# Performance work log

Measured on AMD Instinct MI355X. Metric: run time of the kernel, lower is better.

The kernel has to match this reference:

```python
import jax, jax.numpy as jnp
import numpy as np

B, S, D, H = 2, 2048, 2048, 16
HD = D // H


def setup_inputs() -> dict:
    key = jax.random.key(0)
    ks = jax.random.split(key, 11)
    scale = 1.0 / np.sqrt(D)
    causal = jnp.tril(jnp.ones((S, S), dtype=bool))
    attention_mask = jnp.broadcast_to(causal, (B, H, S, S))
    return {
        "queries": jax.random.normal(ks[0], (B, S, D), dtype=jnp.float32),
        "keys": jax.random.normal(ks[1], (B, S, D), dtype=jnp.float32),
        "values": jax.random.normal(ks[2], (B, S, D), dtype=jnp.float32),
        "attention_mask": attention_mask,
        "wq": jax.random.normal(ks[3], (D, D), dtype=jnp.float32) * scale,
        "bq": jax.random.normal(ks[4], (D,), dtype=jnp.float32) * 0.01,
        "wk": jax.random.normal(ks[5], (D, D), dtype=jnp.float32) * scale,
        "bk": jax.random.normal(ks[6], (D,), dtype=jnp.float32) * 0.01,
        "wv": jax.random.normal(ks[7], (D, D), dtype=jnp.float32) * scale,
        "bv": jax.random.normal(ks[8], (D,), dtype=jnp.float32) * 0.01,
        "wo": jax.random.normal(ks[9], (D, D), dtype=jnp.float32) * scale,
        "bo": jax.random.normal(ks[10], (D,), dtype=jnp.float32) * 0.01,
    }


def _split_heads(x):
    # (B, S, D) -> (B, H, S, HD)
    b, s, _ = x.shape
    return x.reshape(b, s, H, HD).transpose(0, 2, 1, 3)


def reference(queries, keys, values, attention_mask, wq, bq, wk, bk, wv, bv, wo, bo):
    # Linear layers (torch convention: x @ W.T + b)
    q = _split_heads(queries @ wq.T + bq)   # (B, H, S, HD)
    k = _split_heads(keys @ wk.T + bk)
    v = _split_heads(values @ wv.T + bv)

    inv_sqrt_d = 1.0 / jnp.sqrt(jnp.asarray(HD, dtype=q.dtype))
    scores = jnp.einsum('bhqd,bhkd->bhqk', q, k) * inv_sqrt_d  # (B, H, S, S)
    scores = jnp.where(attention_mask, scores, jnp.asarray(-jnp.inf, dtype=scores.dtype))
    probs = jax.nn.softmax(scores, axis=-1)
    out = jnp.einsum('bhqk,bhkd->bhqd', probs, v)              # (B, H, S, HD)

    out = out.transpose(0, 2, 1, 3).reshape(queries.shape[0], queries.shape[1], D)
    return out @ wo.T + bo
```

## Files before the change

kernel.cpp:

```cpp
#include <hip/hip_runtime.h>
#include <hip/hip_bf16.h>

typedef unsigned short u16;
typedef __bf16 bf16x8 __attribute__((ext_vector_type(8)));
typedef short  short8 __attribute__((ext_vector_type(8)));
typedef float  f32x4  __attribute__((ext_vector_type(4)));
typedef float  f32x16 __attribute__((ext_vector_type(16)));
typedef u16    u16x4  __attribute__((ext_vector_type(4)));
typedef unsigned uintx2 __attribute__((ext_vector_type(2)));

#define BB 2
#define SS 2048
#define DD 2048
#define HH 16
#define HDIM 128
#define MM (BB * SS)
#define KSCALE 0.12752039505554602f

static __device__ __forceinline__ f32x4 mfma16(short8 a, short8 b, f32x4 c) {
    return __builtin_amdgcn_mfma_f32_16x16x32_bf16(
        __builtin_bit_cast(bf16x8, a), __builtin_bit_cast(bf16x8, b), c, 0, 0, 0);
}

static __device__ __forceinline__ f32x16 mfma32(short8 a, short8 b, f32x16 c) {
    return __builtin_amdgcn_mfma_f32_32x32x16_bf16(
        __builtin_bit_cast(bf16x8, a), __builtin_bit_cast(bf16x8, b), c, 0, 0, 0);
}

static __device__ __forceinline__ u16 f2bf(float f) {
    union { float f; unsigned u; } v; v.f = f;
    unsigned r = v.u + 0x7fffu + ((v.u >> 16) & 1u);
    return (u16)(r >> 16);
}

static __device__ __forceinline__ float bf2f(u16 v) {
    union { unsigned u; float f; } t; t.u = ((unsigned)v) << 16;
    return t.f;
}

static __device__ __forceinline__ unsigned cvtpk(float lo, float hi) {
    unsigned r;
    asm("v_cvt_pk_bf16_f32 %0, %1, %2" : "=v"(r) : "v"(lo), "v"(hi));
    return r;
}

static __device__ __forceinline__ void plswap(unsigned &a, unsigned &b) {
    asm("v_permlane32_swap_b32 %0, %1" : "+v"(a), "+v"(b));
}

static __device__ __forceinline__ uint4 pack8(float4 a, float4 b) {
    uint4 o;
    o.x = (unsigned)f2bf(a.x) | ((unsigned)f2bf(a.y) << 16);
    o.y = (unsigned)f2bf(a.z) | ((unsigned)f2bf(a.w) << 16);
    o.z = (unsigned)f2bf(b.x) | ((unsigned)f2bf(b.y) << 16);
    o.w = (unsigned)f2bf(b.z) | ((unsigned)f2bf(b.w) << 16);
    return o;
}

static __device__ __forceinline__ void gload_lds16(const u16* g, u16* l) {
    __builtin_amdgcn_global_load_lds(
        (const __attribute__((address_space(1))) unsigned int*)g,
        (__attribute__((address_space(3))) unsigned int*)l, 16, 0, 0);
}

__global__ __launch_bounds__(256) void conv_all(
    const float* __restrict__ q, const float* __restrict__ k, const float* __restrict__ v,
    const float* __restrict__ wq, const float* __restrict__ wk,
    const float* __restrict__ wv, const float* __restrict__ wo,
    u16* __restrict__ out)
{
    constexpr int n1 = MM * DD / 8;
    constexpr int nw = DD * DD / 8;
    constexpr int total = 3 * n1 + 4 * nw;
    const int stride = gridDim.x * blockDim.x;
    for (int i = blockIdx.x * blockDim.x + threadIdx.x; i < total; i += stride) {
        const float* s; int j = i; float sc = 1.f;
        if (j < n1)            { s = q; }
        else if (j < 2 * n1)   { s = k;  j -= n1; }
        else if (j < 3 * n1)   { s = v;  j -= 2 * n1; }
        else {
            j -= 3 * n1;
            if (j < nw)        { s = wq; sc = KSCALE; }
            else if (j < 2*nw) { s = wk; j -= nw; }
            else if (j < 3*nw) { s = wv; j -= 2 * nw; }
            else               { s = wo; j -= 3 * nw; }
        }
        const float4* sp = (const float4*)s + (size_t)j * 2;
        float4 a = sp[0], bb2 = sp[1];
        a.x *= sc; a.y *= sc; a.z *= sc; a.w *= sc;
        bb2.x *= sc; bb2.y *= sc; bb2.z *= sc; bb2.w *= sc;
        ((uint4*)out)[i] = pack8(a, bb2);
    }
}

__global__ __launch_bounds__(256, 3) void gemm_qkv(
    const u16* __restrict__ A0, const u16* __restrict__ W0,
    const float* __restrict__ bq, const float* __restrict__ bk,
    const float* __restrict__ bv, u16* __restrict__ C0)
{
    __shared__ u16 S[128 * 132];
    u16* Al = S;
    u16* Bl = S + 4096;

    const int z = blockIdx.z;
    const u16* A  = A0 + (size_t)z * MM * DD;
    const u16* Wb = W0 + (size_t)z * DD * DD;
    const float* bias = (z == 0) ? bq : (z == 1 ? bk : bv);
    const float bsc = (z == 0) ? KSCALE : 1.f;

    const int tid = threadIdx.x;
    const int lane = tid & 63;
    const int lg = lane >> 4, li = lane & 15;
    const int wid = tid >> 6;
    const int brow = blockIdx.x * 128, bcol = blockIdx.y * 128;
    const int wm = wid >> 1, wn = wid & 1;

    const int srow = tid >> 2;
    const int scol = (tid & 3) * 8;

    const f32x4 zero = {0.f, 0.f, 0.f, 0.f};
    f32x4 acc[4][4];
#pragma unroll
    for (int i = 0; i < 4; ++i)
#pragma unroll
        for (int j = 0; j < 4; ++j) acc[i][j] = zero;

    const u16* aptr = A  + (size_t)(brow + srow) * DD + scol;
    const u16* bptr = Wb + (size_t)(bcol + srow) * DD + scol;
    const size_t half = (size_t)64 * DD;

    for (int kt = 0; kt < DD; kt += 32) {
        gload_lds16(aptr + kt,        &Al[tid * 8]);
        gload_lds16(aptr + half + kt, &Al[2048 + tid * 8]);
        gload_lds16(bptr + kt,        &Bl[tid * 8]);
        gload_lds16(bptr + half + kt, &Bl[2048 + tid * 8]);
        __syncthreads();

        short8 af[4], bf[4];
#pragma unroll
        for (int mi = 0; mi < 4; ++mi)
            af[mi] = *(const short8*)(&Al[(wm * 64 + mi * 16 + li) * 32 + lg * 8]);
#pragma unroll
        for (int ni = 0; ni < 4; ++ni)
            bf[ni] = *(const short8*)(&Bl[(wn * 64 + ni * 16 + li) * 32 + lg * 8]);
#pragma unroll
        for (int mi = 0; mi < 4; ++mi)
#pragma unroll
            for (int ni = 0; ni < 4; ++ni)
                acc[mi][ni] = mfma16(af[mi], bf[ni], acc[mi][ni]);
        __syncthreads();
    }

    if (z == 2) {
        u16* Cl = S;
#pragma unroll
        for (int ni = 0; ni < 4; ++ni) {
            const int cc = wn * 64 + ni * 16 + li;
            const float bvv = bias[bcol + cc];
#pragma unroll
            for (int mi = 0; mi < 4; ++mi)
#pragma unroll
                for (int r = 0; r < 4; ++r) {
                    const int rr = wm * 64 + mi * 16 + lg * 4 + r;
                    Cl[cc * 132 + rr] = f2bf(acc[mi][ni][r] + bvv);
                }
        }
        __syncthreads();
        const int row = tid >> 1;
        const int hcol = (tid & 1) * 64;
        u16* dst = C0 + (size_t)2 * MM * DD + (size_t)(bcol + row) * MM + brow + hcol;
#pragma unroll
        for (int c = 0; c < 8; ++c)
            *(short8*)(dst + c * 8) = *(const short8*)(&Cl[row * 132 + hcol + c * 8]);
    } else {
        u16* Cp = C0 + (size_t)z * MM * DD;
#pragma unroll
        for (int ni = 0; ni < 4; ++ni) {
            const int col = bcol + wn * 64 + ni * 16 + li;
            const float bvv = bias[col] * bsc;
#pragma unroll
            for (int mi = 0; mi < 4; ++mi)
#pragma unroll
                for (int r = 0; r < 4; ++r) {
                    const int row = brow + wm * 64 + mi * 16 + lg * 4 + r;
                    Cp[(size_t)row * DD + col] = f2bf(acc[mi][ni][r] + bvv);
                }
        }
    }
}

__global__ __launch_bounds__(256) void gemm_out(
    const u16* __restrict__ A, const u16* __restrict__ Wb,
    const float* __restrict__ bias, float* __restrict__ Cp)
{
    __shared__ u16 Al[128 * 32];
    __shared__ u16 Bl[128 * 32];

    const int tid = threadIdx.x;
    const int lane = tid & 63;
    const int lg = lane >> 4, li = lane & 15;
    const int wid = tid >> 6;
    const int brow = blockIdx.x * 128, bcol = blockIdx.y * 128;
    const int wm = wid >> 1, wn = wid & 1;

    const f32x4 zero = {0.f, 0.f, 0.f, 0.f};
    f32x4 acc[4][4];
#pragma unroll
    for (int i = 0; i < 4; ++i)
#pragma unroll
        for (int j = 0; j < 4; ++j) acc[i][j] = zero;

    const int srow = tid >> 2;
    const int scol = (tid & 3) * 8;
    const u16* aptr = A  + (size_t)(brow + srow) * DD + scol;
    const u16* bptr = Wb + (size_t)(bcol + srow) * DD + scol;
    const size_t half = (size_t)64 * DD;

    for (int kt = 0; kt < DD; kt += 32) {
        gload_lds16(aptr + kt,        &Al[tid * 8]);
        gload_lds16(aptr + half + kt, &Al[2048 + tid * 8]);
        gload_lds16(bptr + kt,        &Bl[tid * 8]);
        gload_lds16(bptr + half + kt, &Bl[2048 + tid * 8]);
        __syncthreads();

        short8 af[4], bf[4];
#pragma unroll
        for (int mi = 0; mi < 4; ++mi)
            af[mi] = *(const short8*)(&Al[(wm * 64 + mi * 16 + li) * 32 + lg * 8]);
#pragma unroll
        for (int ni = 0; ni < 4; ++ni)
            bf[ni] = *(const short8*)(&Bl[(wn * 64 + ni * 16 + li) * 32 + lg * 8]);
#pragma unroll
        for (int mi = 0; mi < 4; ++mi)
#pragma unroll
            for (int ni = 0; ni < 4; ++ni)
                acc[mi][ni] = mfma16(af[mi], bf[ni], acc[mi][ni]);
        __syncthreads();
    }

#pragma unroll
    for (int ni = 0; ni < 4; ++ni) {
        const int col = bcol + wn * 64 + ni * 16 + li;
        const float bvv = bias[col];
#pragma unroll
        for (int mi = 0; mi < 4; ++mi)
#pragma unroll
            for (int r = 0; r < 4; ++r) {
                const int row = brow + wm * 64 + mi * 16 + lg * 4 + r;
                Cp[(size_t)row * DD + col] = acc[mi][ni][r] + bvv;
            }
    }
}

__global__ __launch_bounds__(256) void flash_attn(
    const u16* __restrict__ Q, const u16* __restrict__ Kp,
    const u16* __restrict__ Vt, u16* __restrict__ O,
    u16* __restrict__ PartO, float* __restrict__ PartML)
{
    __shared__ u16 lds[16384];
    u16* Kl = lds;
    u16* Vl = lds + 8192;

    const int tid = threadIdx.x;
    const int wid = tid >> 6, lane = tid & 63;
    const int l5 = lane & 31;
    const int hi = lane >> 5;

    const int lin = (int)blockIdx.x + 51 * ((int)blockIdx.y + 16 * (int)blockIdx.z);
    const int xcd = lin & 7;
    const int idx = lin >> 3;
    const int grp = xcd + 8 * (idx & 3);
    const int f   = idx >> 2;
    const int b = grp >> 4, h = grp & 15;

    int qt = 15, rem = f, C;
    for (;;) { C = (2 * qt + 7) / 6; if (rem < C) break; rem -= C; --qt; }
    const int ch = rem;
    const int T = 2 * qt + 2;
    const int j0 = ch * T / C;
    const int j1 = (ch + 1) * T / C;
    const int qbase = qt * 128 + wid * 32;
    const int qg = qbase + l5;

    const int rK0 = tid >> 4, wK0 = tid & 15;
    const int bK0 = ((wK0 * 16) ^ ((rK0 & 7) << 4)) >> 1;
    const int rV0 = tid >> 3, wV0 = tid & 7;
    const int bV0 = ((wV0 * 16) ^ ((rV0 & 7) << 4)) >> 1;
    const u16* kbase = Kp + (size_t)(b * SS + rK0) * DD + h * HDIM + bK0;
    const u16* vbase = Vt + (size_t)(h * HDIM + rV0) * MM + b * SS + bV0;

    short8 qf[8];
    {
        const u16* qp0 = Q + (size_t)(b * SS + qg) * DD + h * HDIM + hi * 8;
#pragma unroll
        for (int ks = 0; ks < 8; ++ks)
            qf[ks] = *(const short8*)(qp0 + ks * 16);
    }

    float m_r = -__builtin_inff(), l_r = 0.f;
    f32x16 accO[4];
#pragma unroll
    for (int d = 0; d < 4; ++d) accO[d] = (f32x16)(0.f);

    for (int j = j0; j < j1; ++j) {
#pragma unroll
        for (int i_ = 0; i_ < 4; ++i_) {
            gload_lds16(kbase + (size_t)(j * 64 + i_ * 16) * DD, &Kl[(i_ * 256 + tid) * 8]);
            gload_lds16(vbase + (size_t)(i_ * 32) * MM + j * 64, &Vl[(i_ * 256 + tid) * 8]);
        }
        __syncthreads();

        if (j * 64 <= qbase + 31) {
            f32x16 accS[2];
            accS[0] = (f32x16)(0.f); accS[1] = (f32x16)(0.f);
            __builtin_amdgcn_s_setprio(1);
#pragma unroll
            for (int ks = 0; ks < 8; ++ks) {
#pragma unroll
                for (int kvb = 0; kvb < 2; ++kvb) {
                    const int row = kvb * 32 + l5;
                    const int e = (ks * 16 + hi * 8) ^ ((row & 7) << 3);
                    short8 kf = *(const short8*)(&Kl[row * 128 + e]);
                    accS[kvb] = mfma32(kf, qf[ks], accS[kvb]);
                }
            }
            __builtin_amdgcn_s_setprio(0);

            const bool domask = (j * 64 + 63 > qbase);
            float rmax = -__builtin_inff();
            if (domask) {
#pragma unroll
                for (int kvb = 0; kvb < 2; ++kvb)
#pragma unroll
                    for (int r = 0; r < 16; ++r) {
                        float t = accS[kvb][r];
                        const int kv = j * 64 + kvb * 32 + (r & 3) + 8 * (r >> 2) + 4 * hi;
                        if (kv > qg) t = -__builtin_inff();
                        accS[kvb][r] = t;
                        rmax = fmaxf(rmax, t);
                    }
            } else {
#pragma unroll
                for (int kvb = 0; kvb < 2; ++kvb)
#pragma unroll
                    for (int r = 0; r < 16; ++r)
                        rmax = fmaxf(rmax, accS[kvb][r]);
            }
            rmax = fmaxf(rmax, __shfl_xor(rmax, 32, 64));

            if (!__all(rmax - m_r <= 11.5f)) {
                const float mn = fmaxf(m_r, rmax);
                const float sf = exp2f(m_r - mn);
                m_r = mn;
                l_r *= sf;
#pragma unroll
                for (int db = 0; db < 4; ++db) accO[db] = accO[db] * sf;
            }

            float ls = 0.f;
#pragma unroll
            for (int kvb = 0; kvb < 2; ++kvb)
#pragma unroll
                for (int r = 0; r < 16; ++r) {
                    const float e = exp2f(accS[kvb][r] - m_r);
                    accS[kvb][r] = e;
                    ls += e;
                }
            ls += __shfl_xor(ls, 32, 64);
            l_r += ls;

            __builtin_amdgcn_s_setprio(1);
#pragma unroll
            for (int ks = 0; ks < 4; ++ks) {
                const int kvb = ks >> 1;
                const int r0 = (ks & 1) * 8;
                unsigned x0 = cvtpk(accS[kvb][r0 + 0], accS[kvb][r0 + 1]);
                unsigned y0 = cvtpk(accS[kvb][r0 + 2], accS[kvb][r0 + 3]);
                unsigned x1 = cvtpk(accS[kvb][r0 + 4], accS[kvb][r0 + 5]);
                unsigned y1 = cvtpk(accS[kvb][r0 + 6], accS[kvb][r0 + 7]);
                plswap(x0, x1);
                plswap(y0, y1);
                union { unsigned u[4]; short8 s; } pf;
                pf.u[0] = x0; pf.u[1] = y0; pf.u[2] = x1; pf.u[3] = y1;
#pragma unroll
                for (int db = 0; db < 4; ++db) {
                    const int row = db * 32 + l5;
                    const int e = (ks * 16 + hi * 8) ^ ((row & 7) << 3);
                    short8 vf = *(const short8*)(&Vl[row * 64 + e]);
                    accO[db] = mfma32(vf, pf.s, accO[db]);
                }
            }
            __builtin_amdgcn_s_setprio(0);
        }
        __syncthreads();
    }

    if (C > 1) {
        int sbase = 0;
        for (int q2 = 3; q2 < qt; ++q2) sbase += (2 * q2 + 7) / 6;
        const int pslot = grp * 48 + sbase + ch;
        u16* po = PartO + (size_t)pslot * 16384 + (size_t)(wid * 32 + l5) * 128;
#pragma unroll
        for (int db = 0; db < 4; ++db)
#pragma unroll
            for (int g = 0; g < 4; ++g) {
                const int d0 = db * 32 + g * 8 + hi * 4;
                uintx2 pk;
                pk.x = cvtpk(accO[db][g * 4 + 0], accO[db][g * 4 + 1]);
                pk.y = cvtpk(accO[db][g * 4 + 2], accO[db][g * 4 + 3]);
                *(uintx2*)(po + d0) = pk;
            }
        if (lane < 32) {
            float* ml = PartML + (size_t)pslot * 256;
            ml[wid * 32 + l5]       = m_r;
            ml[128 + wid * 32 + l5] = l_r;
        }
    } else {
        const float linv = 1.f / l_r;
        u16* Wl = lds + wid * 4096;
#pragma unroll
        for (int db = 0; db < 4; ++db)
#pragma unroll
            for (int g = 0; g < 4; ++g) {
                const int d0 = db * 32 + g * 8 + hi * 4;
                uintx2 pk;
                pk.x = cvtpk(accO[db][g * 4 + 0] * linv, accO[db][g * 4 + 1] * linv);
                pk.y = cvtpk(accO[db][g * 4 + 2] * linv, accO[db][g * 4 + 3] * linv);
                *(uintx2*)(&Wl[l5 * 128 + (d0 ^ ((l5 & 7) << 4))]) = pk;
            }
        const int q_l = lane >> 1;
        const int d0r = (lane & 1) * 64;
        u16* op = O + (size_t)(b * SS + qt * 128 + wid * 32 + q_l) * DD + h * HDIM + d0r;
#pragma unroll
        for (int c = 0; c < 8; ++c) {
            short8 vv = *(const short8*)(&Wl[q_l * 128 + ((d0r + c * 8) ^ ((q_l & 7) << 4))]);
            *(short8*)(op + c * 8) = vv;
        }
    }
}

__global__ __launch_bounds__(256) void attn_combine(
    const u16* __restrict__ PartO, const float* __restrict__ PartML,
    u16* __restrict__ O)
{
    const int qt = 3 + (int)blockIdx.x;
    const int h = blockIdx.y, b = blockIdx.z;
    const int nch = (2 * qt + 7) / 6;
    int sbase = 0;
    for (int q2 = 3; q2 < qt; ++q2) sbase += (2 * q2 + 7) / 6;
    const int pbase = (b * HH + h) * 48 + sbase;

    const int tid = threadIdx.x;
    const int q = tid & 127;
    const int d0 = (tid >> 7) * 64;

    float mc[6], lc[6];
#pragma unroll
    for (int c = 0; c < 6; ++c) {
        if (c < nch) {
            mc[c] = PartML[(size_t)(pbase + c) * 256 + q];
            lc[c] = PartML[(size_t)(pbase + c) * 256 + 128 + q];
        } else { mc[c] = -__builtin_inff(); lc[c] = 0.f; }
    }
    float M = mc[0];
#pragma unroll
    for (int c = 1; c < 6; ++c) M = fmaxf(M, mc[c]);
    float wc[6], L = 0.f;
#pragma unroll
    for (int c = 0; c < 6; ++c) { wc[c] = exp2f(mc[c] - M); L += wc[c] * lc[c]; }
    const float Linv = 1.f / L;

    float acc[64];
#pragma unroll
    for (int i = 0; i < 64; ++i) acc[i] = 0.f;
#pragma unroll
    for (int c = 0; c < 6; ++c) {
        if (c < nch) {
            const float w = wc[c] * Linv;
            const u16* po = PartO + (size_t)(pbase + c) * 16384 + (size_t)q * 128 + d0;
#pragma unroll
            for (int i = 0; i < 64; ++i)
                acc[i] += w * bf2f(po[i]);
        }
    }

    u16* op = O + (size_t)(b * SS + qt * 128 + q) * DD + h * HDIM + d0;
#pragma unroll
    for (int j = 0; j < 8; ++j) {
        short8 vv;
#pragma unroll
        for (int e = 0; e < 8; ++e) vv[e] = (short)f2bf(acc[j * 8 + e]);
        *(short8*)(op + j * 8) = vv;
    }
}

extern "C" void kernel_launch(void* const* d_in, const int* in_sizes, int n_in,
                              void* d_out, int out_size, void* d_ws, size_t ws_size,
                              hipStream_t stream)
{
    const float* queries = (const float*)d_in[0];
    const float* keys    = (const float*)d_in[1];
    const float* values  = (const float*)d_in[2];
    const float* wq = (const float*)d_in[4];
    const float* bq = (const float*)d_in[5];
    const float* wk = (const float*)d_in[6];
    const float* bk = (const float*)d_in[7];
    const float* wv = (const float*)d_in[8];
    const float* bv = (const float*)d_in[9];
    const float* wo = (const float*)d_in[10];
    const float* bo = (const float*)d_in[11];

    const int NMD = MM * DD;
    const int NWW = DD * DD;

    u16* qb  = (u16*)d_ws;
    u16* wqb = qb  + (size_t)3 * NMD;
    u16* wob = wqb + (size_t)3 * NWW;
    u16* qw  = wob + (size_t)NWW;
    u16* aw  = qw  + (size_t)3 * NMD;
    u16*   partO  = qb;
    float* partML = (float*)wqb;
    (void)in_sizes; (void)n_in; (void)out_size; (void)ws_size;

    dim3 blk(256);
    dim3 gridC(2048);
    dim3 gridQKV(MM / 128, DD / 128, 3);
    dim3 gridO(MM / 128, DD / 128);
    dim3 gridA(51, HH, BB);
    dim3 gridX(13, HH, BB);

    conv_all<<<gridC, blk, 0, stream>>>(queries, keys, values, wq, wk, wv, wo, qb);
    gemm_qkv<<<gridQKV, blk, 0, stream>>>(qb, wqb, bq, bk, bv, qw);
    flash_attn<<<gridA, blk, 0, stream>>>(qw, qw + (size_t)NMD, qw + (size_t)2 * NMD, aw,
                                          partO, partML);
    attn_combine<<<gridX, blk, 0, stream>>>(partO, partML, aw);
    gemm_out<<<gridO, blk, 0, stream>>>(aw, wob, bo, (float*)d_out);
}
```

Baseline: 333.2 us.

## Load K and V fragments directly from global memory in flash attention, dropping LDS staging

The flash attention loop no longer stages K and V tiles cooperatively into shared memory with barriers. Each wave now reads its K and V MFMA fragments straight from global memory, and KV blocks that are fully masked are skipped with an early continue. This removes the two block-wide syncs per iteration and the LDS traffic. In exchange the four waves of a block, which share the same K/V tile, each fetch it separately, so they rely on L1/L2 for reuse, and the 16-byte per-lane global loads with strided rows may coalesce poorly.

```diff
diff --git a/kernel.cpp b/kernel.cpp
--- a/kernel.cpp
+++ b/kernel.cpp
@@ -258,8 +258,6 @@
     u16* __restrict__ PartO, float* __restrict__ PartML)
 {
     __shared__ u16 lds[16384];
-    u16* Kl = lds;
-    u16* Vl = lds + 8192;
 
     const int tid = threadIdx.x;
     const int wid = tid >> 6, lane = tid & 63;
@@ -282,12 +280,8 @@
     const int qbase = qt * 128 + wid * 32;
     const int qg = qbase + l5;
 
-    const int rK0 = tid >> 4, wK0 = tid & 15;
-    const int bK0 = ((wK0 * 16) ^ ((rK0 & 7) << 4)) >> 1;
-    const int rV0 = tid >> 3, wV0 = tid & 7;
-    const int bV0 = ((wV0 * 16) ^ ((rV0 & 7) << 4)) >> 1;
-    const u16* kbase = Kp + (size_t)(b * SS + rK0) * DD + h * HDIM + bK0;
-    const u16* vbase = Vt + (size_t)(h * HDIM + rV0) * MM + b * SS + bV0;
+    const u16* kb0 = Kp + (size_t)(b * SS + l5) * DD + h * HDIM + hi * 8;
+    const u16* vb0 = Vt + (size_t)(h * HDIM + l5) * MM + b * SS + hi * 8;
 
     short8 qf[8];
     {
@@ -303,96 +297,86 @@
     for (int d = 0; d < 4; ++d) accO[d] = (f32x16)(0.f);
 
     for (int j = j0; j < j1; ++j) {
-#pragma unroll
-        for (int i_ = 0; i_ < 4; ++i_) {
-            gload_lds16(kbase + (size_t)(j * 64 + i_ * 16) * DD, &Kl[(i_ * 256 + tid) * 8]);
-            gload_lds16(vbase + (size_t)(i_ * 32) * MM + j * 64, &Vl[(i_ * 256 + tid) * 8]);
-        }
-        __syncthreads();
-
-        if (j * 64 <= qbase + 31) {
-            f32x16 accS[2];
-            accS[0] = (f32x16)(0.f); accS[1] = (f32x16)(0.f);
-            __builtin_amdgcn_s_setprio(1);
-#pragma unroll
-            for (int ks = 0; ks < 8; ++ks) {
-#pragma unroll
-                for (int kvb = 0; kvb < 2; ++kvb) {
-                    const int row = kvb * 32 + l5;
-                    const int e = (ks * 16 + hi * 8) ^ ((row & 7) << 3);
-                    short8 kf = *(const short8*)(&Kl[row * 128 + e]);
-                    accS[kvb] = mfma32(kf, qf[ks], accS[kvb]);
+        if (j * 64 > qbase + 31) continue;
+
+        const u16* kj = kb0 + (size_t)(j * 64) * DD;
+        f32x16 accS[2];
+        accS[0] = (f32x16)(0.f); accS[1] = (f32x16)(0.f);
+        __builtin_amdgcn_s_setprio(1);
+#pragma unroll
+        for (int ks = 0; ks < 8; ++ks) {
+#pragma unroll
+            for (int kvb = 0; kvb < 2; ++kvb) {
+                short8 kf = *(const short8*)(kj + (size_t)(kvb * 32) * DD + ks * 16);
+                accS[kvb] = mfma32(kf, qf[ks], accS[kvb]);
+            }
+        }
+        __builtin_amdgcn_s_setprio(0);
+
+        const bool domask = (j * 64 + 63 > qbase);
+        float rmax = -__builtin_inff();
+        if (domask) {
+#pragma unroll
+            for (int kvb = 0; kvb < 2; ++kvb)
+#pragma unroll
+                for (int r = 0; r < 16; ++r) {
+                    float t = accS[kvb][r];
+                    const int kv = j * 64 + kvb * 32 + (r & 3) + 8 * (r >> 2) + 4 * hi;
+                    if (kv > qg) t = -__builtin_inff();
+                    accS[kvb][r] = t;
+                    rmax = fmaxf(rmax, t);
                 }
+        } else {
+#pragma unroll
+            for (int kvb = 0; kvb < 2; ++kvb)
+#pragma unroll
+                for (int r = 0; r < 16; ++r)
+                    rmax = fmaxf(rmax, accS[kvb][r]);
+        }
+        rmax = fmaxf(rmax, __shfl_xor(rmax, 32, 64));
+
+        if (!__all(rmax - m_r <= 11.5f)) {
+            const float mn = fmaxf(m_r, rmax);
+            const float sf = exp2f(m_r - mn);
+            m_r = mn;
+            l_r *= sf;
+#pragma unroll
+            for (int db = 0; db < 4; ++db) accO[db] = accO[db] * sf;
+        }
+
+        float ls = 0.f;
+#pragma unroll
+        for (int kvb = 0; kvb < 2; ++kvb)
+#pragma unroll
+            for (int r = 0; r < 16; ++r) {
+                const float e = exp2f(accS[kvb][r] - m_r);
+                accS[kvb][r] = e;
+                ls += e;
             }
-            __builtin_amdgcn_s_setprio(0);
-
-            const bool domask = (j * 64 + 63 > qbase);
-            float rmax = -__builtin_inff();
-            if (domask) {
-#pragma unroll
-                for (int kvb = 0; kvb < 2; ++kvb)
-#pragma unroll
-                    for (int r = 0; r < 16; ++r) {
-                        float t = accS[kvb][r];
-                        const int kv = j * 64 + kvb * 32 + (r & 3) + 8 * (r >> 2) + 4 * hi;
-                        if (kv > qg) t = -__builtin_inff();
-                        accS[kvb][r] = t;
-                        rmax = fmaxf(rmax, t);
-                    }
-            } else {
-#pragma unroll
-                for (int kvb = 0; kvb < 2; ++kvb)
-#pragma unroll
-                    for (int r = 0; r < 16; ++r)
-                        rmax = fmaxf(rmax, accS[kvb][r]);
+        ls += __shfl_xor(ls, 32, 64);
+        l_r += ls;
+
+        const u16* vj = vb0 + j * 64;
+        __builtin_amdgcn_s_setprio(1);
+#pragma unroll
+        for (int ks = 0; ks < 4; ++ks) {
+            const int kvb = ks >> 1;
+            const int r0 = (ks & 1) * 8;
+            unsigned x0 = cvtpk(accS[kvb][r0 + 0], accS[kvb][r0 + 1]);
+            unsigned y0 = cvtpk(accS[kvb][r0 + 2], accS[kvb][r0 + 3]);
+            unsigned x1 = cvtpk(accS[kvb][r0 + 4], accS[kvb][r0 + 5]);
+            unsigned y1 = cvtpk(accS[kvb][r0 + 6], accS[kvb][r0 + 7]);
+            plswap(x0, x1);
+            plswap(y0, y1);
+            union { unsigned u[4]; short8 s; } pf;
+            pf.u[0] = x0; pf.u[1] = y0; pf.u[2] = x1; pf.u[3] = y1;
+#pragma unroll
+            for (int db = 0; db < 4; ++db) {
+                short8 vf = *(const short8*)(vj + (size_t)(db * 32) * MM + ks * 16);
+                accO[db] = mfma32(vf, pf.s, accO[db]);
             }
-            rmax = fmaxf(rmax, __shfl_xor(rmax, 32, 64));
-
-            if (!__all(rmax - m_r <= 11.5f)) {
-                const float mn = fmaxf(m_r, rmax);
-                const float sf = exp2f(m_r - mn);
-                m_r = mn;
-                l_r *= sf;
-#pragma unroll
-                for (int db = 0; db < 4; ++db) accO[db] = accO[db] * sf;
-            }
-
-            float ls = 0.f;
-#pragma unroll
-            for (int kvb = 0; kvb < 2; ++kvb)
-#pragma unroll
-                for (int r = 0; r < 16; ++r) {
-                    const float e = exp2f(accS[kvb][r] - m_r);
-                    accS[kvb][r] = e;
-                    ls += e;
-                }
-            ls += __shfl_xor(ls, 32, 64);
-            l_r += ls;
-
-            __builtin_amdgcn_s_setprio(1);
-#pragma unroll
-            for (int ks = 0; ks < 4; ++ks) {
-                const int kvb = ks >> 1;
-                const int r0 = (ks & 1) * 8;
-                unsigned x0 = cvtpk(accS[kvb][r0 + 0], accS[kvb][r0 + 1]);
-                unsigned y0 = cvtpk(accS[kvb][r0 + 2], accS[kvb][r0 + 3]);
-                unsigned x1 = cvtpk(accS[kvb][r0 + 4], accS[kvb][r0 + 5]);
-                unsigned y1 = cvtpk(accS[kvb][r0 + 6], accS[kvb][r0 + 7]);
-                plswap(x0, x1);
-                plswap(y0, y1);
-                union { unsigned u[4]; short8 s; } pf;
-                pf.u[0] = x0; pf.u[1] = y0; pf.u[2] = x1; pf.u[3] = y1;
-#pragma unroll
-                for (int db = 0; db < 4; ++db) {
-                    const int row = db * 32 + l5;
-                    const int e = (ks * 16 + hi * 8) ^ ((row & 7) << 3);
-                    short8 vf = *(const short8*)(&Vl[row * 64 + e]);
-                    accO[db] = mfma32(vf, pf.s, accO[db]);
-                }
-            }
-            __builtin_amdgcn_s_setprio(0);
-        }
-        __syncthreads();
+        }
+        __builtin_amdgcn_s_setprio(0);
     }
 
     if (C > 1) {
```

Result: slower. 385.9 us (+15.8%).
